# Optimization experiments

Hardware: AMD Instinct MI355X
Metric: run time of the kernel (lower is better)

The kernel has to match this reference:

```python
import jax, jax.numpy as jnp
import numpy as np

GROUPS = 4
ITER_N = 5


def conv1x1(x, w, b=None):
    # x: (B,C,N,W), w: (O,C)
    y = jnp.einsum('oc,bcnw->bonw', w, x)
    if b is not None:
        y = y + b[None, :, None, None]
    return y


def instance_norm(x, eps=1e-3):
    mu = x.mean(axis=(2, 3), keepdims=True)
    var = x.var(axis=(2, 3), keepdims=True)
    return (x - mu) * jax.lax.rsqrt(var + eps)


def batch_norm(x, g, b, eps=1e-5):
    mu = x.mean(axis=(0, 2, 3), keepdims=True)
    var = x.var(axis=(0, 2, 3), keepdims=True)
    return (x - mu) * jax.lax.rsqrt(var + eps) * g[None, :, None, None] + b[None, :, None, None]


def group_norm(x, g, b, groups=GROUPS, eps=1e-5):
    B, C, N, W = x.shape
    xg = x.reshape(B, groups, C // groups, N, W)
    mu = xg.mean(axis=(2, 3, 4), keepdims=True)
    var = xg.var(axis=(2, 3, 4), keepdims=True)
    xn = ((xg - mu) * jax.lax.rsqrt(var + eps)).reshape(B, C, N, W)
    return xn * g[None, :, None, None] + b[None, :, None, None]


def ns_sqrtm(A, iterN=ITER_N):
    # A: (..., d, d) SPD. MPNCOV Newton-Schulz matrix square root.
    d = A.shape[-1]
    I = jnp.eye(d, dtype=A.dtype)
    trA = jnp.trace(A, axis1=-2, axis2=-1)[..., None, None]
    An = A / trA
    ZY = 0.5 * (3.0 * I - An)
    Y = An @ ZY
    Z = ZY
    for _ in range(iterN - 2):  # fixed small loop over NS iterations
        ZY = 0.5 * (3.0 * I - Z @ Y)
        Y = Y @ ZY
        Z = ZY @ Z
    ZY = 0.5 * (Y @ (3.0 * I - Z @ Y))
    return ZY * jnp.sqrt(trA)


def covar_attn(feat):
    # feat: (B,C,N,W); per-group covariance pooling + sqrtm + channel reweight
    B, C, N, W = feat.shape
    d = C // GROUPS
    M = N * W
    f = feat.reshape(B, GROUPS, d, M)
    fc = f - f.mean(axis=-1, keepdims=True)
    cov = jnp.einsum('bgim,bgjm->bgij', fc, fc) / M  # == x I_hat x^T
    sq = ns_sqrtm(cov)
    s = sq.mean(axis=-2)  # torch.mean(cov_mat_sqrt, 1): mean over rows -> (B,G,d)
    return s.reshape(B, C, 1, 1) * feat


def setup_inputs() -> dict:
    key = jax.random.key(0)
    ks = jax.random.split(key, 4)
    B, C, N, W = 32, 128, 4000, 1
    scale = 1.0 / np.sqrt(C)
    return {
        'x': jax.random.normal(ks[0], (B, C, N, W), jnp.float32),
        'w_linear': jax.random.normal(ks[1], (C, C), jnp.float32) * scale,
        'gn_gamma': jnp.ones((C,), jnp.float32),
        'gn_beta': jnp.zeros((C,), jnp.float32),
        'bn1_g': jnp.ones((C,), jnp.float32),
        'bn1_b': jnp.zeros((C,), jnp.float32),
        'conv1_w': jax.random.normal(ks[2], (C, C), jnp.float32) * scale,
        'conv1_b': jnp.zeros((C,), jnp.float32),
        'bn2_g': jnp.ones((C,), jnp.float32),
        'bn2_b': jnp.zeros((C,), jnp.float32),
        'conv2_w': jax.random.normal(ks[3], (C, C), jnp.float32) * scale,
        'conv2_b': jnp.zeros((C,), jnp.float32),
    }


def reference(x, w_linear, gn_gamma, gn_beta, bn1_g, bn1_b, conv1_w, conv1_b, bn2_g, bn2_b, conv2_w, conv2_b):
    feat = conv1x1(x, w_linear)
    feat_attn = covar_attn(feat)
    y = group_norm(feat_attn + x, gn_gamma, gn_beta)
    # PointCN residual block (inchannel == outchannel -> identity shortcut)
    h = jax.nn.relu(batch_norm(instance_norm(y), bn1_g, bn1_b))
    h = conv1x1(h, conv1_w, conv1_b)
    h = jax.nn.relu(batch_norm(instance_norm(h), bn2_g, bn2_b))
    h = conv1x1(h, conv2_w, conv2_b)
    return h + y
```

## Files before the change

### kernel.cpp

```cpp
#include <hip/hip_runtime.h>

constexpr int Bn = 32;
constexpr int Cn = 128;
constexpr int Mn = 4000;
constexpr int Gn = 4;
constexpr int Dn = 32;
constexpr float GN_EPS = 1e-5f;
constexpr float IN_EPS = 1e-3f;
constexpr float BN_EPS = 1e-5f;

typedef __attribute__((ext_vector_type(8))) short bf16x8;
typedef __attribute__((ext_vector_type(4))) float f32x4;
typedef __attribute__((ext_vector_type(16))) float f32x16;

__device__ __forceinline__ float bf2f(ushort u) {
    union { unsigned int u; float f; } v;
    v.u = ((unsigned int)u) << 16;
    return v.f;
}
__device__ __forceinline__ ushort f2bf(float f) {
    union { float f; unsigned int u; } v;
    v.f = f;
    unsigned int r = v.u + 0x7FFFu + ((v.u >> 16) & 1u);
    return (ushort)(r >> 16);
}

__global__ void prep_w3(const float* __restrict__ w0, const float* __restrict__ w1,
                        const float* __restrict__ w2, ushort* __restrict__ wb) {
    const int i = blockIdx.x * 256 + threadIdx.x;
    const int which = i >> 14;
    const int off = i & 16383;
    const float v = (which == 0) ? w0[off] : (which == 1) ? w1[off] : w2[off];
    wb[i] = f2bf(v);
}

__launch_bounds__(256)
__global__ void prep_xt(const float* __restrict__ x, ushort* __restrict__ xt) {
    __shared__ float tl[128 * 33];
    const int mb = blockIdx.x * 32, b = blockIdx.y;
    const int tid = threadIdx.x;
    const int mi = tid & 31, cg = tid >> 5;
#pragma unroll
    for (int p = 0; p < 16; ++p) {
        const int ci = cg + 8 * p;
        tl[ci * 33 + mi] = x[((size_t)b * Cn + ci) * Mn + mb + mi];
    }
    __syncthreads();
#pragma unroll
    for (int q = 0; q < 2; ++q) {
        const int row = (tid >> 4) + 16 * q;
        const int c8 = (tid & 15) * 8;
        bf16x8 v;
#pragma unroll
        for (int e = 0; e < 8; ++e)
            v[e] = (short)f2bf(tl[(c8 + e) * 33 + row]);
        *(bf16x8*)(xt + ((size_t)b * Mn + mb + row) * Cn + c8) = v;
    }
}

constexpr int WPAD = 136;
constexpr int EP0  = 132;

__launch_bounds__(256, 2)
__global__ void mgemm0_cov(const ushort* __restrict__ Wb,
                           const ushort* __restrict__ src,
                           ushort* __restrict__ dst_bf,
                           float* __restrict__ sf, float* __restrict__ sf2,
                           float* __restrict__ sfxp,
                           float* __restrict__ sxp, float* __restrict__ sx2p,
                           float* __restrict__ covp)
{
    __shared__ ushort Wl[128 * WPAD];
    __shared__ ushort El[64 * EP0];
    const int b = blockIdx.y;
    const int mb0 = blockIdx.x * 256;
    const int tid = threadIdx.x;
    const int wv = tid >> 6, l = tid & 63;
    const int li = l & 15, lg = l >> 4;

#pragma unroll
    for (int p = 0; p < 8; ++p) {
        const int u = tid + 256 * p;
        const int o = u >> 4, c8 = (u & 15) * 8;
        *(bf16x8*)&Wl[o * WPAD + c8] = *(const bf16x8*)(Wb + (size_t)o * 128 + c8);
    }
    __syncthreads();

    f32x16 cacc;
#pragma unroll
    for (int i = 0; i < 16; ++i) cacc[i] = 0.f;
    float s1a[8] = {}, s2a[8] = {}, s3a[8] = {}, s4a[8] = {}, s5a[8] = {};

    const int c8s = (tid & 15) * 8;
    const int cg = wv * 32 + (l & 31);
    const int kb8 = (l >> 5) * 8;

#pragma unroll 1
    for (int t = 0; t < 4; ++t) {
        const int mb = mb0 + t * 64;
        const int ma = mb + wv * 16 + li;
        const bool mok = ma < Mn;
        const size_t qrow = ((size_t)b * Mn + (mok ? ma : (Mn - 1))) * Cn;

        bf16x8 fr[4];
#pragma unroll
        for (int kb = 0; kb < 4; ++kb)
            fr[kb] = *(const bf16x8*)(src + qrow + kb * 32 + 8 * lg);

        f32x4 acc[8];
#pragma unroll
        for (int j = 0; j < 8; ++j)
#pragma unroll
            for (int r = 0; r < 4; ++r) acc[j][r] = 0.f;

#pragma unroll
        for (int kb = 0; kb < 4; ++kb) {
            const int cl = kb * 32 + 8 * lg;
#pragma unroll
            for (int j = 0; j < 8; ++j) {
                const bf16x8 bj = *(const bf16x8*)&Wl[(j * 16 + li) * WPAD + cl];
                acc[j] = __builtin_amdgcn_mfma_f32_16x16x32_bf16(fr[kb], bj, acc[j], 0, 0, 0);
            }
        }

        __syncthreads();
#pragma unroll
        for (int j = 0; j < 8; ++j) {
            const int o = j * 16 + li;
#pragma unroll
            for (int r = 0; r < 4; ++r) {
                const int ml = wv * 16 + lg * 4 + r;
                El[ml * EP0 + o] = (mb + ml < Mn) ? f2bf(acc[j][r]) : (ushort)0;
            }
        }
        __syncthreads();

#pragma unroll
        for (int p = 0; p < 4; ++p) {
            const int row = (tid >> 4) + 16 * p;
            const int m = mb + row;
            const bf16x8 v8 = *(const bf16x8*)&El[row * EP0 + c8s];
            if (m < Mn) {
                const size_t q = ((size_t)b * Mn + m) * Cn + c8s;
                *(bf16x8*)(dst_bf + q) = v8;
                const bf16x8 x8 = *(const bf16x8*)(src + q);
#pragma unroll
                for (int e = 0; e < 8; ++e) {
                    const float f = bf2f((ushort)v8[e]);
                    const float xv = bf2f((ushort)x8[e]);
                    s1a[e] += f;
                    s2a[e] = fmaf(f, f, s2a[e]);
                    s3a[e] = fmaf(f, xv, s3a[e]);
                    s4a[e] += xv;
                    s5a[e] = fmaf(xv, xv, s5a[e]);
                }
            }
        }

#pragma unroll
        for (int ks = 0; ks < 4; ++ks) {
            bf16x8 fgr;
#pragma unroll
            for (int e = 0; e < 8; ++e)
                fgr[e] = (short)El[(ks * 16 + kb8 + e) * EP0 + cg];
            cacc = __builtin_amdgcn_mfma_f32_32x32x16_bf16(fgr, fgr, cacc, 0, 0, 0);
        }
    }

    __syncthreads();
#pragma unroll
    for (int e = 0; e < 8; ++e) {
        s1a[e] += __shfl_xor(s1a[e], 16); s1a[e] += __shfl_xor(s1a[e], 32);
        s2a[e] += __shfl_xor(s2a[e], 16); s2a[e] += __shfl_xor(s2a[e], 32);
        s3a[e] += __shfl_xor(s3a[e], 16); s3a[e] += __shfl_xor(s3a[e], 32);
        s4a[e] += __shfl_xor(s4a[e], 16); s4a[e] += __shfl_xor(s4a[e], 32);
        s5a[e] += __shfl_xor(s5a[e], 16); s5a[e] += __shfl_xor(s5a[e], 32);
    }
    float* red = (float*)El;
    if (l < 16) {
#pragma unroll
        for (int e = 0; e < 8; ++e) {
            red[(wv * 16 + l) * 40 + e]      = s1a[e];
            red[(wv * 16 + l) * 40 + 8 + e]  = s2a[e];
            red[(wv * 16 + l) * 40 + 16 + e] = s3a[e];
            red[(wv * 16 + l) * 40 + 24 + e] = s4a[e];
            red[(wv * 16 + l) * 40 + 32 + e] = s5a[e];
        }
    }
    __syncthreads();
    if (tid < 128) {
        const int oc = tid >> 3, e = tid & 7;
        const int o = oc * 8 + e;
        float t1 = 0.f, t2 = 0.f, t3 = 0.f, t4 = 0.f, t5 = 0.f;
#pragma unroll
        for (int w = 0; w < 4; ++w) {
            t1 += red[(w * 16 + oc) * 40 + e];
            t2 += red[(w * 16 + oc) * 40 + 8 + e];
            t3 += red[(w * 16 + oc) * 40 + 16 + e];
            t4 += red[(w * 16 + oc) * 40 + 24 + e];
            t5 += red[(w * 16 + oc) * 40 + 32 + e];
        }
        atomicAdd(&sf[b * Cn + o], t1);
        atomicAdd(&sf2[b * Cn + o], t2);
        atomicAdd(&sfxp[b * Cn + o], t3);
        atomicAdd(&sxp[b * Cn + o], t4);
        atomicAdd(&sx2p[b * Cn + o], t5);
    }
    float* cvb = covp + (size_t)(b * Gn + wv) * (Dn * Dn);
#pragma unroll
    for (int reg = 0; reg < 16; ++reg) {
        const int i = (reg & 3) + 8 * (reg >> 2) + 4 * (l >> 5);
        const int j = l & 31;
        atomicAdd(&cvb[i * Dn + j], cacc[reg]);
    }
}

constexpr int EPAD = 68;

template <int MODE>
__launch_bounds__(256, 4)
__global__ void mgemm_kernel(const ushort* __restrict__ Wb,
                             const ushort* __restrict__ src,
                             const ushort* __restrict__ xsrc,
                             ushort* __restrict__ dst_bf,
                             float* __restrict__ dst_f32,
                             const float* __restrict__ bias,
                             const float* __restrict__ sarr,
                             const float* __restrict__ tA,
                             const float* __restrict__ tB,
                             const float* __restrict__ Ayc,
                             const float* __restrict__ Byc,
                             ushort* __restrict__ ybuf,
                             float* __restrict__ sum1,
                             float* __restrict__ sum2)
{
    __shared__ ushort Wl[64 * WPAD];
    __shared__ float coefLDS[640];
    const int b = blockIdx.z;
    const int ob = blockIdx.y * 64;
    const int mb = blockIdx.x * 64;
    const int tid = threadIdx.x;
    const int wv = tid >> 6, l = tid & 63;
    const int li = l & 15, lg = l >> 4;
    const bool writeY = (blockIdx.y == 0);

#pragma unroll
    for (int p = 0; p < 4; ++p) {
        const int u = tid + 256 * p;
        const int row = u >> 4, c8 = (u & 15) * 8;
        *(bf16x8*)&Wl[row * WPAD + c8] = *(const bf16x8*)(Wb + (size_t)(ob + row) * 128 + c8);
    }
    {
        const int ncoef = (MODE == 1) ? 640 : 256;
        for (int idx = tid; idx < ncoef; idx += 256) {
            const int arr = idx >> 7, c = idx & 127;
            float v;
            switch (arr) {
                case 0: v = tA[b * Cn + c]; break;
                case 1: v = tB[b * Cn + c]; break;
                case 2: v = sarr[b * Cn + c]; break;
                case 3: v = Ayc[b * Cn + c]; break;
                default: v = Byc[b * Cn + c]; break;
            }
            coefLDS[idx] = v;
        }
    }
    __syncthreads();

    f32x4 acc[4];
#pragma unroll
    for (int j = 0; j < 4; ++j)
#pragma unroll
        for (int r = 0; r < 4; ++r) acc[j][r] = 0.f;

    const int ma = mb + wv * 16 + li;
    const bool mok = ma < Mn;
    const size_t qrow = ((size_t)b * Mn + (mok ? ma : (Mn - 1))) * Cn;

    bf16x8 fr[4], xr[4];
#pragma unroll
    for (int kb = 0; kb < 4; ++kb) {
        const int cl = kb * 32 + 8 * lg;
        fr[kb] = *(const bf16x8*)(src + qrow + cl);
        if (MODE == 1) xr[kb] = *(const bf16x8*)(xsrc + qrow + cl);
    }

#pragma unroll
    for (int kb = 0; kb < 4; ++kb) {
        const int cl = kb * 32 + 8 * lg;
        bf16x8 af;
        if (MODE == 1) {
            const float4 a0 = *(const float4*)&coefLDS[0 + cl];
            const float4 a1 = *(const float4*)&coefLDS[0 + cl + 4];
            const float4 b0 = *(const float4*)&coefLDS[128 + cl];
            const float4 b1 = *(const float4*)&coefLDS[128 + cl + 4];
            const float4 s0 = *(const float4*)&coefLDS[256 + cl];
            const float4 s1 = *(const float4*)&coefLDS[256 + cl + 4];
            const float tAv[8] = {a0.x,a0.y,a0.z,a0.w,a1.x,a1.y,a1.z,a1.w};
            const float tBv[8] = {b0.x,b0.y,b0.z,b0.w,b1.x,b1.y,b1.z,b1.w};
            const float svv[8] = {s0.x,s0.y,s0.z,s0.w,s1.x,s1.y,s1.z,s1.w};
            float vv[8];
#pragma unroll
            for (int e = 0; e < 8; ++e) {
                vv[e] = fmaf(svv[e], bf2f((ushort)fr[kb][e]), bf2f((ushort)xr[kb][e]));
                af[e] = (short)f2bf(fmaxf(fmaf(tAv[e], vv[e], tBv[e]), 0.f));
            }
            if (writeY && mok) {
                const float4 y0 = *(const float4*)&coefLDS[384 + cl];
                const float4 y1 = *(const float4*)&coefLDS[384 + cl + 4];
                const float4 z0 = *(const float4*)&coefLDS[512 + cl];
                const float4 z1 = *(const float4*)&coefLDS[512 + cl + 4];
                const float ayv[8] = {y0.x,y0.y,y0.z,y0.w,y1.x,y1.y,y1.z,y1.w};
                const float byv[8] = {z0.x,z0.y,z0.z,z0.w,z1.x,z1.y,z1.z,z1.w};
                bf16x8 y8;
#pragma unroll
                for (int e = 0; e < 8; ++e)
                    y8[e] = (short)f2bf(fmaf(ayv[e], vv[e], byv[e]));
                *(bf16x8*)(ybuf + qrow + cl) = y8;
            }
        } else {
            const float4 a0 = *(const float4*)&coefLDS[0 + cl];
            const float4 a1 = *(const float4*)&coefLDS[0 + cl + 4];
            const float4 b0 = *(const float4*)&coefLDS[128 + cl];
            const float4 b1 = *(const float4*)&coefLDS[128 + cl + 4];
            const float tAv[8] = {a0.x,a0.y,a0.z,a0.w,a1.x,a1.y,a1.z,a1.w};
            const float tBv[8] = {b0.x,b0.y,b0.z,b0.w,b1.x,b1.y,b1.z,b1.w};
#pragma unroll
            for (int e = 0; e < 8; ++e)
                af[e] = (short)f2bf(fmaxf(fmaf(tAv[e], bf2f((ushort)fr[kb][e]), tBv[e]), 0.f));
        }
#pragma unroll
        for (int j = 0; j < 4; ++j) {
            const bf16x8 bj = *(const bf16x8*)&Wl[(j * 16 + li) * WPAD + cl];
            acc[j] = __builtin_amdgcn_mfma_f32_16x16x32_bf16(af, bj, acc[j], 0, 0, 0);
        }
    }

    if constexpr (MODE == 1) {
        __syncthreads();
        ushort* El = Wl;
#pragma unroll
        for (int j = 0; j < 4; ++j) {
            const int o = j * 16 + li;
            const float bv = bias[ob + o];
#pragma unroll
            for (int r = 0; r < 4; ++r) {
                const int ml = wv * 16 + lg * 4 + r;
                El[ml * EPAD + o] = f2bf(acc[j][r] + bv);
            }
        }
        __syncthreads();
        const int c8l = (tid & 7) * 8;
        float s1a[8] = {}, s2a[8] = {};
#pragma unroll
        for (int p = 0; p < 2; ++p) {
            const int row = (tid >> 3) + 32 * p;
            const int m = mb + row;
            const bf16x8 v8 = *(const bf16x8*)&El[row * EPAD + c8l];
            if (m < Mn) {
                *(bf16x8*)(dst_bf + ((size_t)b * Mn + m) * Cn + ob + c8l) = v8;
#pragma unroll
                for (int e = 0; e < 8; ++e) {
                    const float f = bf2f((ushort)v8[e]);
                    s1a[e] += f;
                    s2a[e] = fmaf(f, f, s2a[e]);
                }
            }
        }
#pragma unroll
        for (int e = 0; e < 8; ++e) {
            s1a[e] += __shfl_xor(s1a[e], 8);  s2a[e] += __shfl_xor(s2a[e], 8);
            s1a[e] += __shfl_xor(s1a[e], 16); s2a[e] += __shfl_xor(s2a[e], 16);
            s1a[e] += __shfl_xor(s1a[e], 32); s2a[e] += __shfl_xor(s2a[e], 32);
        }
        __syncthreads();
        float* red = coefLDS;
        if (l < 8) {
#pragma unroll
            for (int e = 0; e < 8; ++e) {
                red[wv * 128 + l * 8 + e] = s1a[e];
                red[wv * 128 + 64 + l * 8 + e] = s2a[e];
            }
        }
        __syncthreads();
        if (tid < 128) {
            const int which = tid >> 6, ol = tid & 63;
            const float v = red[0 * 128 + which * 64 + ol] + red[1 * 128 + which * 64 + ol] +
                            red[2 * 128 + which * 64 + ol] + red[3 * 128 + which * 64 + ol];
            atomicAdd((which ? sum2 : sum1) + b * Cn + ob + ol, v);
        }
    } else {
        __syncthreads();
        ushort* El = Wl;
        float* TR = (float*)(Wl + 64 * EPAD);
#pragma unroll
        for (int p = 0; p < 2; ++p) {
            const int row = (tid >> 3) + 32 * p;
            const int c8l = (tid & 7) * 8;
            bf16x8 yv;
#pragma unroll
            for (int e = 0; e < 8; ++e) yv[e] = 0;
            if (mb + row < Mn)
                yv = *(const bf16x8*)(ybuf + ((size_t)b * Mn + mb + row) * Cn + ob + c8l);
            *(bf16x8*)&El[row * EPAD + c8l] = yv;
        }
        __syncthreads();
#pragma unroll
        for (int j = 0; j < 4; ++j) {
            const int o = j * 16 + li;
            const float bv = bias[ob + o];
#pragma unroll
            for (int r = 0; r < 4; ++r) {
                const int ml = wv * 16 + lg * 4 + r;
                acc[j][r] += bv + bf2f(El[ml * EPAD + o]);
            }
        }
#pragma unroll
        for (int h = 0; h < 2; ++h) {
#pragma unroll
            for (int jj = 0; jj < 2; ++jj) {
                const int j = h * 2 + jj;
#pragma unroll
                for (int r = 0; r < 4; ++r) {
                    const int ml = wv * 16 + lg * 4 + r;
                    TR[(jj * 16 + li) * EPAD + ml] = acc[j][r];
                }
            }
            __syncthreads();
#pragma unroll
            for (int p = 0; p < 2; ++p) {
                const int u = tid + 256 * p;
                const int ol = u >> 4, q = u & 15;
                const int m = mb + 4 * q;
                if (m < Mn) {
                    const f32x4 v = *(const f32x4*)&TR[ol * EPAD + 4 * q];
                    *(f32x4*)(dst_f32 + ((size_t)b * Cn + ob + h * 32 + ol) * Mn + m) = v;
                }
            }
            __syncthreads();
        }
    }
}

__device__ __forceinline__ void mm32(float (*A)[33], float (*Bm)[33],
                                     float (*O)[33], int ei, int ej0)
{
    float a0 = 0.f, a1 = 0.f, a2 = 0.f, a3 = 0.f;
#pragma unroll
    for (int k = 0; k < 32; ++k) {
        const float a = A[ei][k];
        a0 = fmaf(a, Bm[k][ej0 + 0], a0);
        a1 = fmaf(a, Bm[k][ej0 + 1], a1);
        a2 = fmaf(a, Bm[k][ej0 + 2], a2);
        a3 = fmaf(a, Bm[k][ej0 + 3], a3);
    }
    O[ei][ej0 + 0] = a0;
    O[ei][ej0 + 1] = a1;
    O[ei][ej0 + 2] = a2;
    O[ei][ej0 + 3] = a3;
    __syncthreads();
}

__launch_bounds__(256)
__global__ void sqrtm_kernel(const float* __restrict__ cov,
                             const float* __restrict__ sf,
                             float* __restrict__ sout)
{
    __shared__ float b0[32][33], b1[32][33], b2[32][33], b3[32][33];
    __shared__ float sh_tr, sh_scale;
    const int bg = blockIdx.x;
    const int b = bg >> 2, g = bg & 3;
    const int tid = threadIdx.x;
    const int ei = (tid * 4) >> 5, ej0 = (tid * 4) & 31;
    const float* cp = cov + (size_t)bg * (Dn * Dn);
    const float* fs = sf + b * Cn + g * Dn;
    const float invM = 1.f / Mn;
    const float mi = fs[ei] * invM;
#pragma unroll
    for (int q = 0; q < 4; ++q)
        b0[ei][ej0 + q] = cp[ei * Dn + ej0 + q] * invM - mi * (fs[ej0 + q] * invM);
    __syncthreads();
    if (tid < 32) {
        float d = b0[tid][tid];
#pragma unroll
        for (int dd = 1; dd < 32; dd <<= 1) d += __shfl_xor(d, dd);
        if (tid == 0) { sh_tr = d; sh_scale = 0.5f * sqrtf(d); }
    }
    __syncthreads();
    const float invtr = 1.f / sh_tr;
#pragma unroll
    for (int q = 0; q < 4; ++q) {
        const float an = b0[ei][ej0 + q] * invtr;
        b0[ei][ej0 + q] = an;
        b1[ei][ej0 + q] = ((ei == ej0 + q) ? 1.5f : 0.f) - 0.5f * an;
    }
    __syncthreads();
    mm32(b0, b1, b2, ei, ej0);
    float (*pY)[33] = b2;
    float (*pZ)[33] = b1;
    float (*pF1)[33] = b0;
    float (*pF2)[33] = b3;
#pragma unroll 1
    for (int it = 0; it < 3; ++it) {
        mm32(pZ, pY, pF1, ei, ej0);
#pragma unroll
        for (int q = 0; q < 4; ++q)
            pF1[ei][ej0 + q] = ((ei == ej0 + q) ? 1.5f : 0.f) - 0.5f * pF1[ei][ej0 + q];
        __syncthreads();
        mm32(pY, pF1, pF2, ei, ej0);
        mm32(pF1, pZ, pY, ei, ej0);
        float (*oldZ)[33] = pZ;
        pZ = pY;
        pY = pF2;
        pF2 = oldZ;
    }
    mm32(pZ, pY, pF1, ei, ej0);
#pragma unroll
    for (int q = 0; q < 4; ++q)
        pF1[ei][ej0 + q] = ((ei == ej0 + q) ? 3.f : 0.f) - pF1[ei][ej0 + q];
    __syncthreads();
    mm32(pY, pF1, pF2, ei, ej0);
    if (tid < 32) {
        float t = 0.f;
#pragma unroll
        for (int i = 0; i < 32; ++i) t += pF2[i][tid];
        sout[b * Cn + g * Dn + tid] = t * sh_scale * (1.f / Dn);
    }
}

__launch_bounds__(1024)
__global__ void coef1_kernel(const float* __restrict__ sf, const float* __restrict__ sf2,
                             const float* __restrict__ sfx, const float* __restrict__ sx,
                             const float* __restrict__ sx2, const float* __restrict__ s,
                             const float* __restrict__ gng, const float* __restrict__ gnb,
                             const float* __restrict__ bn1g, const float* __restrict__ bn1b,
                             float* __restrict__ Ay, float* __restrict__ By,
                             float* __restrict__ Ah, float* __restrict__ Bh)
{
    __shared__ float smv[Bn * Cn];
    __shared__ float sm2[Bn * Cn];
    __shared__ float smu[Bn * Gn], srs[Bn * Gn];
    __shared__ float sV[Cn];
    const int tid = threadIdx.x;
    const float invM = 1.f / Mn;
    for (int p = tid; p < Bn * Cn; p += 1024) {
        const float sv = s[p];
        smv[p] = fmaf(sv, sf[p], sx[p]) * invM;
        sm2[p] = (sv * sv * sf2[p] + 2.f * sv * sfx[p] + sx2[p]) * invM;
    }
    __syncthreads();
    if (tid < Bn * Gn) {
        const int base = tid * Dn;
        float mu = 0.f, e2 = 0.f;
        for (int c = 0; c < Dn; ++c) { mu += smv[base + c]; e2 += sm2[base + c]; }
        mu *= (1.f / Dn); e2 *= (1.f / Dn);
        smu[tid] = mu;
        srs[tid] = rsqrtf(e2 - mu * mu + GN_EPS);
    }
    __syncthreads();
    for (int p = tid; p < Bn * Cn; p += 1024) {
        const int c = p & (Cn - 1);
        const int bg = p >> 5;
        const float ay = srs[bg] * gng[c];
        const float mv = smv[p];
        sm2[p] = ay * ay * (sm2[p] - mv * mv);
    }
    __syncthreads();
    if (tid < Cn) {
        float V = 0.f;
        for (int b = 0; b < Bn; ++b) {
            const float vy = sm2[b * Cn + tid];
            V += vy / (vy + IN_EPS);
        }
        sV[tid] = V * (1.f / Bn);
    }
    __syncthreads();
    for (int p = tid; p < Bn * Cn; p += 1024) {
        const int c = p & (Cn - 1);
        const int bg = p >> 5;
        const float ay = srs[bg] * gng[c];
        const float mv = smv[p];
        const float by = gnb[c] - smu[bg] * ay;
        const float rsin = rsqrtf(sm2[p] + IN_EPS);
        const float ah = ay * rsin * rsqrtf(sV[c] + BN_EPS) * bn1g[c];
        const float bh = bn1b[c] - ah * mv;
        Ay[p] = ay; By[p] = by; Ah[p] = ah; Bh[p] = bh;
    }
}

__launch_bounds__(1024)
__global__ void coef2_kernel(const float* __restrict__ sum1, const float* __restrict__ sum2,
                             const float* __restrict__ bn2g, const float* __restrict__ bn2b,
                             float* __restrict__ A2, float* __restrict__ B2)
{
    __shared__ float svar[Bn * Cn];
    __shared__ float sV[Cn];
    const int tid = threadIdx.x;
    const float invM = 1.f / Mn;
    for (int p = tid; p < Bn * Cn; p += 1024) {
        const float mu = sum1[p] * invM;
        svar[p] = sum2[p] * invM - mu * mu;
    }
    __syncthreads();
    if (tid < Cn) {
        float V = 0.f;
        for (int b = 0; b < Bn; ++b) {
            const float v = svar[b * Cn + tid];
            V += v / (v + IN_EPS);
        }
        sV[tid] = V * (1.f / Bn);
    }
    __syncthreads();
    for (int p = tid; p < Bn * Cn; p += 1024) {
        const int c = p & (Cn - 1);
        const float mu = sum1[p] * invM;
        const float a2 = rsqrtf(svar[p] + IN_EPS) * rsqrtf(sV[c] + BN_EPS) * bn2g[c];
        A2[p] = a2;
        B2[p] = bn2b[c] - a2 * mu;
    }
}

extern "C" void kernel_launch(void* const* d_in, const int* in_sizes, int n_in,
                              void* d_out, int out_size, void* d_ws, size_t ws_size,
                              hipStream_t stream)
{
    const float* x      = (const float*)d_in[0];
    const float* w_lin  = (const float*)d_in[1];
    const float* gn_g   = (const float*)d_in[2];
    const float* gn_b   = (const float*)d_in[3];
    const float* bn1g   = (const float*)d_in[4];
    const float* bn1b   = (const float*)d_in[5];
    const float* conv1w = (const float*)d_in[6];
    const float* conv1b = (const float*)d_in[7];
    const float* bn2g   = (const float*)d_in[8];
    const float* bn2b   = (const float*)d_in[9];
    const float* conv2w = (const float*)d_in[10];
    const float* conv2b = (const float*)d_in[11];
    float* out = (float*)d_out;

    const size_t TS = (size_t)Bn * Mn * Cn;
    ushort* xt    = (ushort*)d_ws;
    ushort* featt = xt + TS;
    ushort* h2t   = featt + TS;
    ushort* ybuf  = h2t + TS;
    ushort* wb1   = ybuf + TS;
    ushort* wb2   = wb1 + Cn * Cn;
    ushort* wb3   = wb2 + Cn * Cn;
    float*  fbase = (float*)(wb3 + Cn * Cn);
    float* sarr = fbase;
    float* Ay   = sarr + Bn * Cn;
    float* By   = Ay + Bn * Cn;
    float* Ah   = By + Bn * Cn;
    float* Bh   = Ah + Bn * Cn;
    float* A2   = Bh + Bn * Cn;
    float* B2   = A2 + Bn * Cn;
    float* zbase = B2 + Bn * Cn;
    float* cov  = zbase;
    float* sf   = cov + Bn * Gn * Dn * Dn;
    float* sf2  = sf + Bn * Cn;
    float* sfx  = sf2 + Bn * Cn;
    float* sx   = sfx + Bn * Cn;
    float* sx2  = sx + Bn * Cn;
    float* sum1 = sx2 + Bn * Cn;
    float* sum2 = sum1 + Bn * Cn;
    const size_t zfloats = (size_t)Bn * Gn * Dn * Dn + 7 * Bn * Cn;

    hipMemsetAsync(zbase, 0, zfloats * sizeof(float), stream);

    prep_w3<<<dim3(192), 256, 0, stream>>>(w_lin, conv1w, conv2w, wb1);
    prep_xt<<<dim3(Mn / 32, Bn), 256, 0, stream>>>(x, xt);

    mgemm0_cov<<<dim3((Mn + 255) / 256, Bn), 256, 0, stream>>>(
        wb1, xt, featt, sf, sf2, sfx, sx, sx2, cov);

    sqrtm_kernel<<<Bn * Gn, 256, 0, stream>>>(cov, sf, sarr);

    coef1_kernel<<<1, 1024, 0, stream>>>(sf, sf2, sfx, sx, sx2, sarr,
                                         gn_g, gn_b, bn1g, bn1b, Ay, By, Ah, Bh);

    const dim3 ggrid((Mn + 63) / 64, 2, Bn);

    mgemm_kernel<1><<<ggrid, 256, 0, stream>>>(
        wb2, featt, xt, h2t, nullptr, conv1b, sarr, Ah, Bh,
        Ay, By, ybuf, sum1, sum2);

    coef2_kernel<<<1, 1024, 0, stream>>>(sum1, sum2, bn2g, bn2b, A2, B2);

    mgemm_kernel<2><<<ggrid, 256, 0, stream>>>(
        wb3, h2t, nullptr, nullptr, out, conv2b, nullptr, A2, B2,
        nullptr, nullptr, ybuf, nullptr, nullptr);
}
```

Measured before the change: 140.5 us.

## Recompute residual y in final GEMM instead of materializing ybuf

The first mgemm stage no longer writes the group-normalized residual y to a bf16 scratch buffer. The final GEMM epilogue instead rebuilds y from featt and xt using the attention scale and the GN coefficients. This trades one full tensor write plus read for two tensor reads and a little extra arithmetic. The launch bounds hint also moves from 4 to 8 blocks per CU, which may cap registers per thread.

After: 139.5 us. About the same (-0.7%).

```diff
diff --git a/kernel.cpp b/kernel.cpp
--- a/kernel.cpp
+++ b/kernel.cpp
@@ -218,7 +218,7 @@
 constexpr int EPAD = 68;
 
 template <int MODE>
-__launch_bounds__(256, 4)
+__launch_bounds__(256, 8)
 __global__ void mgemm_kernel(const ushort* __restrict__ Wb,
                              const ushort* __restrict__ src,
                              const ushort* __restrict__ xsrc,
@@ -230,7 +230,8 @@
                              const float* __restrict__ tB,
                              const float* __restrict__ Ayc,
                              const float* __restrict__ Byc,
-                             ushort* __restrict__ ybuf,
+                             const ushort* __restrict__ yfeat,
+                             const ushort* __restrict__ yxt,
                              float* __restrict__ sum1,
                              float* __restrict__ sum2)
 {
@@ -242,7 +243,6 @@
     const int tid = threadIdx.x;
     const int wv = tid >> 6, l = tid & 63;
     const int li = l & 15, lg = l >> 4;
-    const bool writeY = (blockIdx.y == 0);
 
 #pragma unroll
     for (int p = 0; p < 4; ++p) {
@@ -251,7 +251,7 @@
         *(bf16x8*)&Wl[row * WPAD + c8] = *(const bf16x8*)(Wb + (size_t)(ob + row) * 128 + c8);
     }
     {
-        const int ncoef = (MODE == 1) ? 640 : 256;
+        const int ncoef = (MODE == 1) ? 384 : 640;
         for (int idx = tid; idx < ncoef; idx += 256) {
             const int arr = idx >> 7, c = idx & 127;
             float v;
@@ -299,24 +299,10 @@
             const float tAv[8] = {a0.x,a0.y,a0.z,a0.w,a1.x,a1.y,a1.z,a1.w};
             const float tBv[8] = {b0.x,b0.y,b0.z,b0.w,b1.x,b1.y,b1.z,b1.w};
             const float svv[8] = {s0.x,s0.y,s0.z,s0.w,s1.x,s1.y,s1.z,s1.w};
-            float vv[8];
 #pragma unroll
             for (int e = 0; e < 8; ++e) {
-                vv[e] = fmaf(svv[e], bf2f((ushort)fr[kb][e]), bf2f((ushort)xr[kb][e]));
-                af[e] = (short)f2bf(fmaxf(fmaf(tAv[e], vv[e], tBv[e]), 0.f));
-            }
-            if (writeY && mok) {
-                const float4 y0 = *(const float4*)&coefLDS[384 + cl];
-                const float4 y1 = *(const float4*)&coefLDS[384 + cl + 4];
-                const float4 z0 = *(const float4*)&coefLDS[512 + cl];
-                const float4 z1 = *(const float4*)&coefLDS[512 + cl + 4];
-                const float ayv[8] = {y0.x,y0.y,y0.z,y0.w,y1.x,y1.y,y1.z,y1.w};
-                const float byv[8] = {z0.x,z0.y,z0.z,z0.w,z1.x,z1.y,z1.z,z1.w};
-                bf16x8 y8;
-#pragma unroll
-                for (int e = 0; e < 8; ++e)
-                    y8[e] = (short)f2bf(fmaf(ayv[e], vv[e], byv[e]));
-                *(bf16x8*)(ybuf + qrow + cl) = y8;
+                const float vv = fmaf(svv[e], bf2f((ushort)fr[kb][e]), bf2f((ushort)xr[kb][e]));
+                af[e] = (short)f2bf(fmaxf(fmaf(tAv[e], vv, tBv[e]), 0.f));
             }
         } else {
             const float4 a0 = *(const float4*)&coefLDS[0 + cl];
@@ -393,15 +379,24 @@
         __syncthreads();
         ushort* El = Wl;
         float* TR = (float*)(Wl + 64 * EPAD);
+        const int c8l = (tid & 7) * 8;
 #pragma unroll
         for (int p = 0; p < 2; ++p) {
             const int row = (tid >> 3) + 32 * p;
-            const int c8l = (tid & 7) * 8;
             bf16x8 yv;
 #pragma unroll
             for (int e = 0; e < 8; ++e) yv[e] = 0;
-            if (mb + row < Mn)
-                yv = *(const bf16x8*)(ybuf + ((size_t)b * Mn + mb + row) * Cn + ob + c8l);
+            if (mb + row < Mn) {
+                const size_t q = ((size_t)b * Mn + mb + row) * Cn + ob + c8l;
+                const bf16x8 f8 = *(const bf16x8*)(yfeat + q);
+                const bf16x8 x8 = *(const bf16x8*)(yxt + q);
+#pragma unroll
+                for (int e = 0; e < 8; ++e) {
+                    const int c = ob + c8l + e;
+                    const float vv = fmaf(coefLDS[256 + c], bf2f((ushort)f8[e]), bf2f((ushort)x8[e]));
+                    yv[e] = (short)f2bf(fmaf(coefLDS[384 + c], vv, coefLDS[512 + c]));
+                }
+            }
             *(bf16x8*)&El[row * EPAD + c8l] = yv;
         }
         __syncthreads();
@@ -642,8 +637,7 @@
     ushort* xt    = (ushort*)d_ws;
     ushort* featt = xt + TS;
     ushort* h2t   = featt + TS;
-    ushort* ybuf  = h2t + TS;
-    ushort* wb1   = ybuf + TS;
+    ushort* wb1   = h2t + TS;
     ushort* wb2   = wb1 + Cn * Cn;
     ushort* wb3   = wb2 + Cn * Cn;
     float*  fbase = (float*)(wb3 + Cn * Cn);
@@ -682,11 +676,11 @@
 
     mgemm_kernel<1><<<ggrid, 256, 0, stream>>>(
         wb2, featt, xt, h2t, nullptr, conv1b, sarr, Ah, Bh,
-        Ay, By, ybuf, sum1, sum2);
+        nullptr, nullptr, nullptr, nullptr, sum1, sum2);
 
     coef2_kernel<<<1, 1024, 0, stream>>>(sum1, sum2, bn2g, bn2b, A2, B2);
 
     mgemm_kernel<2><<<ggrid, 256, 0, stream>>>(
-        wb3, h2t, nullptr, nullptr, out, conv2b, nullptr, A2, B2,
-        nullptr, nullptr, ybuf, nullptr, nullptr);
-}
+        wb3, h2t, nullptr, nullptr, out, conv2b, sarr, A2, B2,
+        Ay, By, featt, xt, nullptr, nullptr);
+}
```
